# Performance work log

Measured on AMD Instinct MI355X. Metric: run time of the kernel, lower is better.

Reference implementation:

```python
import jax, jax.numpy as jnp
import numpy as np

H = 1024          # hidden_size
V = 50257         # output_size (vocab)
L = 64            # max_length


def setup_inputs() -> dict:
    key = jax.random.key(0)
    ks = jax.random.split(key, 20)
    s = 0.02
    inp = {
        "input": jax.random.randint(ks[0], (1,), 0, V, dtype=jnp.int64) if jax.config.jax_enable_x64 else jax.random.randint(ks[0], (1,), 0, V, dtype=jnp.int32),
        "hidden": jax.random.normal(ks[1], (2, 1, H), dtype=jnp.float32),
        "encoder_output": jax.random.normal(ks[2], (1, 2 * H), dtype=jnp.float32),
        "encoder_outputs": jax.random.normal(ks[3], (L, 2 * H), dtype=jnp.float32),
        # parameters
        "emb": jax.random.normal(ks[4], (V, H), dtype=jnp.float32) * s,
        "attn_W": jax.random.normal(ks[5], (L, 3 * H), dtype=jnp.float32) * s,
        "attn_b": jnp.zeros((L,), dtype=jnp.float32),
        "comb_W": jax.random.normal(ks[6], (H, 3 * H), dtype=jnp.float32) * s,
        "comb_b": jnp.zeros((H,), dtype=jnp.float32),
        "Wih_f": jax.random.normal(ks[7], (3 * H, H), dtype=jnp.float32) * s,
        "Whh_f": jax.random.normal(ks[8], (3 * H, H), dtype=jnp.float32) * s,
        "bih_f": jnp.zeros((3 * H,), dtype=jnp.float32),
        "bhh_f": jnp.zeros((3 * H,), dtype=jnp.float32),
        "Wih_b": jax.random.normal(ks[9], (3 * H, H), dtype=jnp.float32) * s,
        "Whh_b": jax.random.normal(ks[10], (3 * H, H), dtype=jnp.float32) * s,
        "bih_b": jnp.zeros((3 * H,), dtype=jnp.float32),
        "bhh_b": jnp.zeros((3 * H,), dtype=jnp.float32),
        "out_W": jax.random.normal(ks[11], (V, 2 * H), dtype=jnp.float32) * s,
        "out_b": jnp.zeros((V,), dtype=jnp.float32),
    }
    return inp


def _gru_cell(x, h, Wih, Whh, bih, bhh):
    # PyTorch GRUCell gate math; x, h: (1, H)
    gi = x @ Wih.T + bih                      # (1, 3H)
    gh = h @ Whh.T + bhh                      # (1, 3H)
    ir, iz, inn = jnp.split(gi, 3, axis=1)
    hr, hz, hn = jnp.split(gh, 3, axis=1)
    r = jax.nn.sigmoid(ir + hr)
    z = jax.nn.sigmoid(iz + hz)
    n = jnp.tanh(inn + r * hn)
    return (1.0 - z) * n + z * h


def reference(input, hidden, encoder_output, encoder_outputs,
              emb, attn_W, attn_b, comb_W, comb_b,
              Wih_f, Whh_f, bih_f, bhh_f,
              Wih_b, Whh_b, bih_b, bhh_b,
              out_W, out_b):
    embedded = emb[input]                     # (1, H); dropout is identity in eval
    h0, h1 = hidden[0], hidden[1]             # (1, H) each
    cat3 = jnp.concatenate([embedded, h0, h1], axis=1)          # (1, 3H)
    attn_weights = jax.nn.softmax(cat3 @ attn_W.T + attn_b, axis=1)  # (1, L)
    attn_applied = attn_weights @ encoder_outputs               # (1, 2H)
    comb = jnp.concatenate([embedded, attn_applied], axis=1)    # (1, 3H)
    x = jax.nn.relu(comb @ comb_W.T + comb_b)                   # (1, H)
    hf = _gru_cell(x, h0, Wih_f, Whh_f, bih_f, bhh_f)           # forward dir
    hb = _gru_cell(x, h1, Wih_b, Whh_b, bih_b, bhh_b)           # backward dir (seq_len=1)
    gru_out = jnp.concatenate([hf, hb], axis=1)                 # (1, 2H)
    new_hidden = jnp.stack([hf, hb], axis=0)                    # (2, 1, H)
    log_probs = jax.nn.log_softmax(gru_out @ out_W.T + out_b, axis=1)  # (1, V)
    return (log_probs, new_hidden, attn_weights)
```

## Files before the change

kernel.cpp:

```cpp
#include <hip/hip_runtime.h>
#include <hip/hip_bf16.h>
#include <math.h>

#define H   1024
#define V   50257
#define L   64
#define H2  2048
#define H3  3072

typedef float float4v __attribute__((ext_vector_type(4)));

#define WS_ATTN_LOGITS 0
#define WS_AA          128
#define WS_X           2176
#define WS_GRU         3200
#define WS_LOGITS      5248
#define WS_RED         55552

#define GEMV_BLOCKS 1024
#define GEMV_WAVES  (GEMV_BLOCKS * 4)

__device__ inline float waveReduceSum(float v) {
#pragma unroll
    for (int off = 32; off > 0; off >>= 1) v += __shfl_down(v, off, 64);
    return v;
}
__device__ inline float waveAllMax(float v) {
#pragma unroll
    for (int off = 32; off > 0; off >>= 1) v = fmaxf(v, __shfl_xor(v, off, 64));
    return v;
}
__device__ inline float waveAllSum(float v) {
#pragma unroll
    for (int off = 32; off > 0; off >>= 1) v += __shfl_xor(v, off, 64);
    return v;
}
__device__ inline void lse_combine(float& m, float& s, float m2, float s2) {
    float M = fmaxf(m, m2);
    s = s * expf(m - M) + s2 * expf(m2 - M);
    m = M;
}

__global__ __launch_bounds__(256) void k_attn_logits(
        const int* __restrict__ tok_p, const float* __restrict__ hidden,
        const float* __restrict__ emb, const float* __restrict__ attn_W,
        const float* __restrict__ attn_b, float* __restrict__ ws) {
    int b = blockIdx.x;
    int tid = threadIdx.x;
    int tok = tok_p[0];
    const float4* w4   = (const float4*)(attn_W + (size_t)b * H3);
    const float4* emb4 = (const float4*)(emb + (size_t)tok * H);
    const float4* hid4 = (const float4*)hidden;
    float acc = 0.f;
#pragma unroll
    for (int k = 0; k < 3; ++k) {
        int idx = tid + k * 256;
        float4 c = (idx < 256) ? emb4[idx] : hid4[idx - 256];
        float4 w = w4[idx];
        acc += c.x * w.x + c.y * w.y + c.z * w.z + c.w * w.w;
    }
    __shared__ float red[4];
    float p = waveReduceSum(acc);
    int lane = tid & 63, wid = tid >> 6;
    if (lane == 0) red[wid] = p;
    __syncthreads();
    if (tid == 0) ws[WS_ATTN_LOGITS + b] = red[0] + red[1] + red[2] + red[3] + attn_b[b];
}

__global__ __launch_bounds__(256) void k_softmax_applied(
        const float* __restrict__ eo, float* __restrict__ ws,
        float* __restrict__ d_out) {
    __shared__ float aw[64];
    int tid = threadIdx.x;
    if (tid < 64) {
        float x = ws[WS_ATTN_LOGITS + tid];
        float m = waveAllMax(x);
        float e = expf(x - m);
        float s = waveAllSum(e);
        float w = e / s;
        aw[tid] = w;
        if (blockIdx.x == 0) d_out[V + H2 + tid] = w;
    }
    __syncthreads();
    int j = blockIdx.x * 256 + tid;
    float acc = 0.f;
#pragma unroll 8
    for (int l = 0; l < L; ++l) acc += aw[l] * eo[l * H2 + j];
    ws[WS_AA + j] = acc;
}

__global__ __launch_bounds__(256) void k_comb_relu(
        const int* __restrict__ tok_p, const float* __restrict__ emb,
        const float* __restrict__ comb_W, const float* __restrict__ comb_b,
        float* __restrict__ ws) {
    int tid = threadIdx.x;
    int lane = tid & 63, wid = tid >> 6;
    int r = blockIdx.x * 4 + wid;
    int tok = tok_p[0];
    const float4* emb4 = (const float4*)(emb + (size_t)tok * H);
    const float4* aa4  = (const float4*)(ws + WS_AA);
    const float4v* w4  = (const float4v*)(comb_W + (size_t)r * H3);
    float acc = 0.f;
#pragma unroll
    for (int k = 0; k < 12; ++k) {
        int idx = lane + k * 64;
        float4 c = (idx < 256) ? emb4[idx] : aa4[idx - 256];
        float4v w = __builtin_nontemporal_load(&w4[idx]);
        acc += c.x * w.x + c.y * w.y + c.z * w.z + c.w * w.w;
    }
    acc = waveReduceSum(acc);
    if (lane == 0) ws[WS_X + r] = fmaxf(acc + comb_b[r], 0.f);
}

__global__ __launch_bounds__(256) void k_gru(
        const float* __restrict__ hidden,
        const float* __restrict__ Wih_f, const float* __restrict__ Whh_f,
        const float* __restrict__ bih_f, const float* __restrict__ bhh_f,
        const float* __restrict__ Wih_b, const float* __restrict__ Whh_b,
        const float* __restrict__ bih_b, const float* __restrict__ bhh_b,
        float* __restrict__ d_out, float* __restrict__ ws) {
    int tid = threadIdx.x;
    int lane = tid & 63, wid = tid >> 6;
    int w = blockIdx.x * 4 + wid;
    int dir = w >> 10;
    int i = w & (H - 1);
    const float* Wih = dir ? Wih_b : Wih_f;
    const float* Whh = dir ? Whh_b : Whh_f;
    const float* bih = dir ? bih_b : bih_f;
    const float* bhh = dir ? bhh_b : bhh_f;
    const float* h = hidden + dir * H;
    const float4* x4  = (const float4*)(ws + WS_X);
    const float4* h4  = (const float4*)h;
    const float4v* wi0 = (const float4v*)(Wih + (size_t)i * H);
    const float4v* wi1 = (const float4v*)(Wih + (size_t)(H + i) * H);
    const float4v* wi2 = (const float4v*)(Wih + (size_t)(2 * H + i) * H);
    const float4v* wh0 = (const float4v*)(Whh + (size_t)i * H);
    const float4v* wh1 = (const float4v*)(Whh + (size_t)(H + i) * H);
    const float4v* wh2 = (const float4v*)(Whh + (size_t)(2 * H + i) * H);
    float a0 = 0, a1 = 0, a2 = 0, b0 = 0, b1 = 0, b2 = 0;
#pragma unroll
    for (int k = 0; k < 4; ++k) {
        int idx = lane + k * 64;
        float4 xv = x4[idx], hv = h4[idx];
        float4v u0 = __builtin_nontemporal_load(&wi0[idx]);
        float4v u1 = __builtin_nontemporal_load(&wi1[idx]);
        float4v u2 = __builtin_nontemporal_load(&wi2[idx]);
        float4v v0 = __builtin_nontemporal_load(&wh0[idx]);
        float4v v1 = __builtin_nontemporal_load(&wh1[idx]);
        float4v v2 = __builtin_nontemporal_load(&wh2[idx]);
        a0 += xv.x*u0.x + xv.y*u0.y + xv.z*u0.z + xv.w*u0.w;
        a1 += xv.x*u1.x + xv.y*u1.y + xv.z*u1.z + xv.w*u1.w;
        a2 += xv.x*u2.x + xv.y*u2.y + xv.z*u2.z + xv.w*u2.w;
        b0 += hv.x*v0.x + hv.y*v0.y + hv.z*v0.z + hv.w*v0.w;
        b1 += hv.x*v1.x + hv.y*v1.y + hv.z*v1.z + hv.w*v1.w;
        b2 += hv.x*v2.x + hv.y*v2.y + hv.z*v2.z + hv.w*v2.w;
    }
    a0 = waveReduceSum(a0); a1 = waveReduceSum(a1); a2 = waveReduceSum(a2);
    b0 = waveReduceSum(b0); b1 = waveReduceSum(b1); b2 = waveReduceSum(b2);
    if (lane == 0) {
        float ir = a0 + bih[i],     iz = a1 + bih[H + i], in_ = a2 + bih[2 * H + i];
        float hr = b0 + bhh[i],     hz = b1 + bhh[H + i], hn  = b2 + bhh[2 * H + i];
        float r = 1.f / (1.f + expf(-(ir + hr)));
        float z = 1.f / (1.f + expf(-(iz + hz)));
        float n = tanhf(in_ + r * hn);
        float hv = (1.f - z) * n + z * h[i];
        d_out[V + dir * H + i] = hv;
        ws[WS_GRU + dir * H + i] = hv;
    }
}

__global__ __launch_bounds__(256) void k_gemv_lse(
        const float* __restrict__ out_W, const float* __restrict__ out_b,
        float* __restrict__ ws) {
    int tid = threadIdx.x;
    int lane = tid & 63, wid = tid >> 6;
    int gw = blockIdx.x * 4 + wid;
    const float4* g4 = (const float4*)(ws + WS_GRU);
    float gv[8];
    float4 gtmp[2];
    gtmp[0] = g4[lane];
    gtmp[1] = g4[lane + 64];
    float m = -3.0e38f, s = 0.f;
    for (int v = gw; v < V; v += 2 * GEMV_WAVES) {
        int v2 = v + GEMV_WAVES;
        const float4v* w4  = (const float4v*)(out_W + (size_t)v * H2);
        float acc0 = 0.f, acc1 = 0.f;
#pragma unroll
        for (int k = 0; k < 8; ++k) {
            int idx = lane + k * 64;
            float4 g = g4[idx];
            float4v w = __builtin_nontemporal_load(&w4[idx]);
            acc0 += g.x * w.x + g.y * w.y + g.z * w.z + g.w * w.w;
        }
        if (v2 < V) {
            const float4v* w4b = (const float4v*)(out_W + (size_t)v2 * H2);
#pragma unroll
            for (int k = 0; k < 8; ++k) {
                int idx = lane + k * 64;
                float4 g = g4[idx];
                float4v w = __builtin_nontemporal_load(&w4b[idx]);
                acc1 += g.x * w.x + g.y * w.y + g.z * w.z + g.w * w.w;
            }
        }
        acc0 = waveReduceSum(acc0);
        acc1 = waveReduceSum(acc1);
        if (lane == 0) {
            float logit = acc0 + out_b[v];
            ws[WS_LOGITS + v] = logit;
            float M = fmaxf(m, logit);
            s = s * expf(m - M) + expf(logit - M);
            m = M;
            if (v2 < V) {
                float logit2 = acc1 + out_b[v2];
                ws[WS_LOGITS + v2] = logit2;
                M = fmaxf(m, logit2);
                s = s * expf(m - M) + expf(logit2 - M);
                m = M;
            }
        }
    }
    (void)gv; (void)gtmp;
    __shared__ float mm[4], ss[4];
    if (lane == 0) { mm[wid] = m; ss[wid] = s; }
    __syncthreads();
    if (tid == 0) {
        float M = mm[0], S = ss[0];
        lse_combine(M, S, mm[1], ss[1]);
        lse_combine(M, S, mm[2], ss[2]);
        lse_combine(M, S, mm[3], ss[3]);
        ws[WS_RED + 2 * blockIdx.x]     = M;
        ws[WS_RED + 2 * blockIdx.x + 1] = S;
    }
}

__global__ __launch_bounds__(256) void k_lse_sub(const float* __restrict__ ws,
                                                 float* __restrict__ d_out) {
    int tid = threadIdx.x;
    int lane = tid & 63, wid = tid >> 6;
    float m = -3.0e38f, s = 0.f;
#pragma unroll
    for (int k = 0; k < 4; ++k) {
        int i = tid + k * 256;
        lse_combine(m, s, ws[WS_RED + 2 * i], ws[WS_RED + 2 * i + 1]);
    }
#pragma unroll
    for (int off = 32; off > 0; off >>= 1) {
        float m2 = __shfl_xor(m, off, 64);
        float s2 = __shfl_xor(s, off, 64);
        lse_combine(m, s, m2, s2);
    }
    __shared__ float mm[4], ss[4], Csh;
    if (lane == 0) { mm[wid] = m; ss[wid] = s; }
    __syncthreads();
    if (tid == 0) {
        float M = mm[0], S = ss[0];
        lse_combine(M, S, mm[1], ss[1]);
        lse_combine(M, S, mm[2], ss[2]);
        lse_combine(M, S, mm[3], ss[3]);
        Csh = M + logf(S);
    }
    __syncthreads();
    float C = Csh;
    int v = blockIdx.x * 256 + tid;
    if (v < V) d_out[v] = ws[WS_LOGITS + v] - C;
}

extern "C" void kernel_launch(void* const* d_in, const int* in_sizes, int n_in,
                              void* d_out, int out_size, void* d_ws, size_t ws_size,
                              hipStream_t stream) {
    const int*   tok     = (const int*)  d_in[0];
    const float* hidden  = (const float*)d_in[1];
    const float* enc_outs= (const float*)d_in[3];
    const float* emb     = (const float*)d_in[4];
    const float* attn_W  = (const float*)d_in[5];
    const float* attn_b  = (const float*)d_in[6];
    const float* comb_W  = (const float*)d_in[7];
    const float* comb_b  = (const float*)d_in[8];
    const float* Wih_f   = (const float*)d_in[9];
    const float* Whh_f   = (const float*)d_in[10];
    const float* bih_f   = (const float*)d_in[11];
    const float* bhh_f   = (const float*)d_in[12];
    const float* Wih_b   = (const float*)d_in[13];
    const float* Whh_b   = (const float*)d_in[14];
    const float* bih_b   = (const float*)d_in[15];
    const float* bhh_b   = (const float*)d_in[16];
    const float* out_W   = (const float*)d_in[17];
    const float* out_b   = (const float*)d_in[18];
    float* out = (float*)d_out;
    float* ws  = (float*)d_ws;

    hipLaunchKernelGGL(k_attn_logits, dim3(64), dim3(256), 0, stream,
                       tok, hidden, emb, attn_W, attn_b, ws);
    hipLaunchKernelGGL(k_softmax_applied, dim3(8), dim3(256), 0, stream,
                       enc_outs, ws, out);
    hipLaunchKernelGGL(k_comb_relu, dim3(256), dim3(256), 0, stream,
                       tok, emb, comb_W, comb_b, ws);
    hipLaunchKernelGGL(k_gru, dim3(512), dim3(256), 0, stream,
                       hidden, Wih_f, Whh_f, bih_f, bhh_f,
                       Wih_b, Whh_b, bih_b, bhh_b, out, ws);
    hipLaunchKernelGGL(k_gemv_lse, dim3(GEMV_BLOCKS), dim3(256), 0, stream,
                       out_W, out_b, ws);
    hipLaunchKernelGGL(k_lse_sub, dim3(197), dim3(256), 0, stream, ws, out);
}
```

Baseline: 93.50 us.

## Fuse log-softmax subtract into output GEMV via grid barrier and cache-aware loads

Merges the output-projection GEMV and the final log-softmax subtraction into one kernel. Every block publishes its partial max/sum, then spins on an atomic counter that k_gru resets, so all blocks can compute the global normaliser and write their own logits. Each wave now processes adjacent row pairs. Rows below a cutoff are read with normal loads instead of nontemporal loads, so that part of out_W can stay in the last-level cache across calls. The grid barrier relies on all 1024 blocks being co-resident, which launch_bounds(256,4) is meant to ensure; if they are not, the kernel can deadlock.

```diff
diff --git a/kernel.cpp b/kernel.cpp
--- a/kernel.cpp
+++ b/kernel.cpp
@@ -16,9 +16,11 @@
 #define WS_GRU         3200
 #define WS_LOGITS      5248
 #define WS_RED         55552
+#define WS_CNT         57600
 
 #define GEMV_BLOCKS 1024
 #define GEMV_WAVES  (GEMV_BLOCKS * 4)
+#define VC          20480
 
 __device__ inline float waveReduceSum(float v) {
 #pragma unroll
@@ -119,6 +121,8 @@
         const float* __restrict__ Wih_b, const float* __restrict__ Whh_b,
         const float* __restrict__ bih_b, const float* __restrict__ bhh_b,
         float* __restrict__ d_out, float* __restrict__ ws) {
+    if (blockIdx.x == 0 && threadIdx.x == 0)
+        *(unsigned*)(ws + WS_CNT) = 0u;
     int tid = threadIdx.x;
     int lane = tid & 63, wid = tid >> 6;
     int w = blockIdx.x * 4 + wid;
@@ -169,88 +173,108 @@
     }
 }
 
-__global__ __launch_bounds__(256) void k_gemv_lse(
+__global__ __launch_bounds__(256, 4) void k_gemv_lse_sub(
         const float* __restrict__ out_W, const float* __restrict__ out_b,
-        float* __restrict__ ws) {
+        float* __restrict__ ws, float* __restrict__ d_out) {
     int tid = threadIdx.x;
     int lane = tid & 63, wid = tid >> 6;
     int gw = blockIdx.x * 4 + wid;
     const float4* g4 = (const float4*)(ws + WS_GRU);
-    float gv[8];
-    float4 gtmp[2];
-    gtmp[0] = g4[lane];
-    gtmp[1] = g4[lane + 64];
     float m = -3.0e38f, s = 0.f;
-    for (int v = gw; v < V; v += 2 * GEMV_WAVES) {
-        int v2 = v + GEMV_WAVES;
-        const float4v* w4  = (const float4v*)(out_W + (size_t)v * H2);
+
+#define DOT2_BODY(LD)                                                        \
+    for (int k = 0; k < 8; ++k) {                                            \
+        int idx = lane + k * 64;                                             \
+        float4  g = g4[idx];                                                 \
+        float4v a = LD(&w0[idx]);                                            \
+        float4v b = LD(&w1[idx]);                                            \
+        acc0 += g.x*a.x + g.y*a.y + g.z*a.z + g.w*a.w;                       \
+        acc1 += g.x*b.x + g.y*b.y + g.z*b.z + g.w*b.w;                       \
+    }
+#define LD_PLAIN(p) (*(p))
+#define LD_NT(p)    (__builtin_nontemporal_load(p))
+
+    for (int it = 0; it < 7; ++it) {
+        int p  = gw + it * 4096;
+        int v0 = 2 * p;
+        if (v0 >= V) break;
+        int v1 = v0 + 1;
+        const float4v* w0 = (const float4v*)(out_W + (size_t)v0 * H2);
+        const float4v* w1 = w0 + 512;
         float acc0 = 0.f, acc1 = 0.f;
-#pragma unroll
-        for (int k = 0; k < 8; ++k) {
-            int idx = lane + k * 64;
-            float4 g = g4[idx];
-            float4v w = __builtin_nontemporal_load(&w4[idx]);
-            acc0 += g.x * w.x + g.y * w.y + g.z * w.z + g.w * w.w;
-        }
-        if (v2 < V) {
-            const float4v* w4b = (const float4v*)(out_W + (size_t)v2 * H2);
+        if (v1 < V) {
+            if (v0 < VC) {
+#pragma unroll
+                DOT2_BODY(LD_PLAIN)
+            } else {
+#pragma unroll
+                DOT2_BODY(LD_NT)
+            }
+        } else {
 #pragma unroll
             for (int k = 0; k < 8; ++k) {
                 int idx = lane + k * 64;
-                float4 g = g4[idx];
-                float4v w = __builtin_nontemporal_load(&w4b[idx]);
-                acc1 += g.x * w.x + g.y * w.y + g.z * w.z + g.w * w.w;
+                float4  g = g4[idx];
+                float4v a = LD_NT(&w0[idx]);
+                acc0 += g.x*a.x + g.y*a.y + g.z*a.z + g.w*a.w;
             }
         }
         acc0 = waveReduceSum(acc0);
         acc1 = waveReduceSum(acc1);
         if (lane == 0) {
-            float logit = acc0 + out_b[v];
-            ws[WS_LOGITS + v] = logit;
-            float M = fmaxf(m, logit);
-            s = s * expf(m - M) + expf(logit - M);
+            float l0 = acc0 + out_b[v0];
+            ws[WS_LOGITS + v0] = l0;
+            float M = fmaxf(m, l0);
+            s = s * expf(m - M) + expf(l0 - M);
             m = M;
-            if (v2 < V) {
-                float logit2 = acc1 + out_b[v2];
-                ws[WS_LOGITS + v2] = logit2;
-                M = fmaxf(m, logit2);
-                s = s * expf(m - M) + expf(logit2 - M);
+            if (v1 < V) {
+                float l1 = acc1 + out_b[v1];
+                ws[WS_LOGITS + v1] = l1;
+                M = fmaxf(m, l1);
+                s = s * expf(m - M) + expf(l1 - M);
                 m = M;
             }
         }
     }
-    (void)gv; (void)gtmp;
-    __shared__ float mm[4], ss[4];
+
+    __shared__ float mm[4], ss[4], Csh;
     if (lane == 0) { mm[wid] = m; ss[wid] = s; }
     __syncthreads();
+    unsigned* cnt = (unsigned*)(ws + WS_CNT);
     if (tid == 0) {
         float M = mm[0], S = ss[0];
         lse_combine(M, S, mm[1], ss[1]);
         lse_combine(M, S, mm[2], ss[2]);
         lse_combine(M, S, mm[3], ss[3]);
-        ws[WS_RED + 2 * blockIdx.x]     = M;
-        ws[WS_RED + 2 * blockIdx.x + 1] = S;
-    }
-}
-
-__global__ __launch_bounds__(256) void k_lse_sub(const float* __restrict__ ws,
-                                                 float* __restrict__ d_out) {
-    int tid = threadIdx.x;
-    int lane = tid & 63, wid = tid >> 6;
-    float m = -3.0e38f, s = 0.f;
+        __hip_atomic_store(&ws[WS_RED + 2 * blockIdx.x],     M,
+                           __ATOMIC_RELAXED, __HIP_MEMORY_SCOPE_AGENT);
+        __hip_atomic_store(&ws[WS_RED + 2 * blockIdx.x + 1], S,
+                           __ATOMIC_RELAXED, __HIP_MEMORY_SCOPE_AGENT);
+        __hip_atomic_fetch_add(cnt, 1u, __ATOMIC_RELEASE,
+                               __HIP_MEMORY_SCOPE_AGENT);
+        while (__hip_atomic_load(cnt, __ATOMIC_ACQUIRE,
+                                 __HIP_MEMORY_SCOPE_AGENT) < GEMV_BLOCKS)
+            __builtin_amdgcn_s_sleep(16);
+    }
+    __syncthreads();
+
+    float cm = -3.0e38f, cs = 0.f;
 #pragma unroll
     for (int k = 0; k < 4; ++k) {
         int i = tid + k * 256;
-        lse_combine(m, s, ws[WS_RED + 2 * i], ws[WS_RED + 2 * i + 1]);
+        float pm = __hip_atomic_load(&ws[WS_RED + 2 * i],     __ATOMIC_RELAXED,
+                                     __HIP_MEMORY_SCOPE_AGENT);
+        float ps = __hip_atomic_load(&ws[WS_RED + 2 * i + 1], __ATOMIC_RELAXED,
+                                     __HIP_MEMORY_SCOPE_AGENT);
+        lse_combine(cm, cs, pm, ps);
     }
 #pragma unroll
     for (int off = 32; off > 0; off >>= 1) {
-        float m2 = __shfl_xor(m, off, 64);
-        float s2 = __shfl_xor(s, off, 64);
-        lse_combine(m, s, m2, s2);
-    }
-    __shared__ float mm[4], ss[4], Csh;
-    if (lane == 0) { mm[wid] = m; ss[wid] = s; }
+        float m2 = __shfl_xor(cm, off, 64);
+        float s2 = __shfl_xor(cs, off, 64);
+        lse_combine(cm, cs, m2, s2);
+    }
+    if (lane == 0) { mm[wid] = cm; ss[wid] = cs; }
     __syncthreads();
     if (tid == 0) {
         float M = mm[0], S = ss[0];
@@ -261,8 +285,16 @@
     }
     __syncthreads();
     float C = Csh;
-    int v = blockIdx.x * 256 + tid;
-    if (v < V) d_out[v] = ws[WS_LOGITS + v] - C;
+
+    if (lane < 14) {
+        int it = lane >> 1;
+        int p  = gw + it * 4096;
+        int v  = 2 * p + (lane & 1);
+        if (v < V) d_out[v] = ws[WS_LOGITS + v] - C;
+    }
+#undef DOT2_BODY
+#undef LD_PLAIN
+#undef LD_NT
 }
 
 extern "C" void kernel_launch(void* const* d_in, const int* in_sizes, int n_in,
@@ -298,7 +330,6 @@
     hipLaunchKernelGGL(k_gru, dim3(512), dim3(256), 0, stream,
                        hidden, Wih_f, Whh_f, bih_f, bhh_f,
                        Wih_b, Whh_b, bih_b, bhh_b, out, ws);
-    hipLaunchKernelGGL(k_gemv_lse, dim3(GEMV_BLOCKS), dim3(256), 0, stream,
-                       out_W, out_b, ws);
-    hipLaunchKernelGGL(k_lse_sub, dim3(197), dim3(256), 0, stream, ws, out);
-}
+    hipLaunchKernelGGL(k_gemv_lse_sub, dim3(GEMV_BLOCKS), dim3(256), 0, stream,
+                       out_W, out_b, ws, out);
+}
```

Result: slower. 280.5 us (+200.0%).
